# Performance work log

Hardware: AMD Instinct MI355X
Metric: run time of the kernel (lower is better)

## Reference

```python
import jax, jax.numpy as jnp
import numpy as np

N = 100000
IN_DIM = 512
OUT_DIM = 512


def setup_inputs() -> dict:
    key = jax.random.key(0)
    k1, k2, k3, k4 = jax.random.split(key, 4)
    x = jax.random.normal(k1, (N, IN_DIM), dtype=jnp.float32)
    edge_index = jax.random.randint(k2, (2, N), 0, N, dtype=jnp.int64)
    # Linear params (torch nn.Linear: out = x @ W.T + b)
    bound = 1.0 / np.sqrt(IN_DIM)
    W = jax.random.uniform(k3, (OUT_DIM, IN_DIM), minval=-bound, maxval=bound, dtype=jnp.float32)
    b = jax.random.uniform(k4, (OUT_DIM,), minval=-bound, maxval=bound, dtype=jnp.float32)
    return {"x": x, "edge_index": edge_index, "W": W, "b": b}


def reference(x, edge_index, W, b):
    # out = relu(linear(x))
    out = jax.nn.relu(jnp.einsum('ni,oi->no', x, W) + b)  # [N, OUT_DIM]
    # torch.scatter_add(out, 0, col[:, None], x):
    # index has shape [E, 1] so only column 0 of src (= x) is scattered:
    # out[col[e], 0] += x[e, 0]
    col = edge_index[1].astype(jnp.int32)  # [E], E == N here
    E = col.shape[0]
    out = out.at[col, 0].add(x[:E, 0])
    return out
```

## Files before the change

### kernel.cpp

```cpp
#include <hip/hip_runtime.h>
#include <stdint.h>

#define K_DIM 512
#define N_OUT 512
#define BM 128
#define BN 128
#define BK 64

typedef __bf16 bf16x8 __attribute__((ext_vector_type(8)));
typedef float f32x4 __attribute__((ext_vector_type(4)));
typedef unsigned short ushort8 __attribute__((ext_vector_type(8)));

__device__ inline unsigned short f2bf(float f) {
  unsigned u = __float_as_uint(f);
  u += 0x7fffu + ((u >> 16) & 1u);
  return (unsigned short)(u >> 16);
}

__global__ __launch_bounds__(256) void prep_kernel(const float* __restrict__ W,
                                                   unsigned short* __restrict__ wb,
                                                   float* __restrict__ s,
                                                   int n8w, int M) {
  int i = blockIdx.x * 256 + threadIdx.x;
  if (i < n8w) {
    const float4* sp = (const float4*)W + (size_t)i * 2;
    float4 a = sp[0], c = sp[1];
    ushort8 o;
    o[0] = f2bf(a.x); o[1] = f2bf(a.y); o[2] = f2bf(a.z); o[3] = f2bf(a.w);
    o[4] = f2bf(c.x); o[5] = f2bf(c.y); o[6] = f2bf(c.z); o[7] = f2bf(c.w);
    *(ushort8*)(wb + (size_t)i * 8) = o;
  } else {
    int j = i - n8w;
    if (j < M) s[j] = 0.f;
  }
}

__global__ __launch_bounds__(256) void scatter_s_kernel(const float* __restrict__ x,
                                                        const int* __restrict__ ei,
                                                        float* __restrict__ s, int E) {
  int e = blockIdx.x * 256 + threadIdx.x;
  if (e < E) {
    int c = ei[E + e];
    atomicAdd(s + c, x[(size_t)e * K_DIM]);
  }
}

__global__ __launch_bounds__(256) void gemm_fused2_kernel(
    const float* __restrict__ x, const unsigned short* __restrict__ wb,
    const float* __restrict__ b, const float* __restrict__ s,
    float* __restrict__ out, int M) {
  __shared__ __align__(16) unsigned short Als[2][BM * BK];
  __shared__ __align__(16) unsigned short Bls[2][BN * BK];

  const int tid = threadIdx.x;
  const int lane = tid & 63;
  const int quad = lane >> 4;
  const int l16 = lane & 15;
  const int waveId = tid >> 6;
  const int wm = (waveId >> 1) * 64;
  const int wn = (waveId & 1) * 64;

  const int nwg = gridDim.x * gridDim.y;
  int raw = blockIdx.y * gridDim.x + blockIdx.x;
  int q = nwg >> 3, r = nwg & 7;
  int xcd = raw & 7;
  int wg = (xcd < r ? xcd * (q + 1) : r * (q + 1) + (xcd - r) * q) + (raw >> 3);
  const int blockM = (wg >> 2) * BM;
  const int blockN = (wg & 3) * BN;

  size_t goffA[4], goffB[4];
  int ldsoff[4];
#pragma unroll
  for (int i = 0; i < 4; ++i) {
    int ch = i * 256 + tid;
    int row = ch >> 3;
    int c8 = ch & 7;
    int sc = c8 ^ (row & 7);
    int ga_row = blockM + row;
    if (ga_row > M - 1) ga_row = M - 1;
    goffA[i] = (size_t)ga_row * K_DIM + sc * 8;
    goffB[i] = (size_t)(blockN + row) * K_DIM + sc * 8;
    ldsoff[i] = ch * 8;
  }

  f32x4 acc[4][4] = {};
  float4 a0[4], a1[4];

#pragma unroll
  for (int i = 0; i < 4; ++i) {
    __builtin_amdgcn_global_load_lds(
        (const __attribute__((address_space(1))) void*)(wb + goffB[i]),
        (__attribute__((address_space(3))) void*)(&Bls[0][ldsoff[i]]), 16, 0, 0);
    a0[i] = *(const float4*)(x + goffA[i]);
    a1[i] = *(const float4*)(x + goffA[i] + 4);
  }
#pragma unroll
  for (int i = 0; i < 4; ++i) {
    ushort8 o;
    o[0] = f2bf(a0[i].x); o[1] = f2bf(a0[i].y); o[2] = f2bf(a0[i].z); o[3] = f2bf(a0[i].w);
    o[4] = f2bf(a1[i].x); o[5] = f2bf(a1[i].y); o[6] = f2bf(a1[i].z); o[7] = f2bf(a1[i].w);
    *(ushort8*)(&Als[0][ldsoff[i]]) = o;
  }
  __syncthreads();

  int cur = 0;
  for (int k0 = 0; k0 < K_DIM; k0 += BK) {
    const int nxt = cur ^ 1;
    const bool has_next = (k0 + BK) < K_DIM;

    if (has_next) {
#pragma unroll
      for (int i = 0; i < 4; ++i) {
        __builtin_amdgcn_global_load_lds(
            (const __attribute__((address_space(1))) void*)(wb + goffB[i] + k0 + BK),
            (__attribute__((address_space(3))) void*)(&Bls[nxt][ldsoff[i]]), 16, 0, 0);
      }
#pragma unroll
      for (int i = 0; i < 4; ++i) {
        a0[i] = *(const float4*)(x + goffA[i] + k0 + BK);
        a1[i] = *(const float4*)(x + goffA[i] + k0 + BK + 4);
      }
    }

#pragma unroll
    for (int ss = 0; ss < 2; ++ss) {
      bf16x8 af[4], bfr[4];
#pragma unroll
      for (int mi = 0; mi < 4; ++mi) {
        int rr = wm + mi * 16 + l16;
        int c = (ss * 4 + quad) ^ (rr & 7);
        af[mi] = *(const bf16x8*)(&Als[cur][rr * BK + c * 8]);
      }
#pragma unroll
      for (int ni = 0; ni < 4; ++ni) {
        int rr = wn + ni * 16 + l16;
        int c = (ss * 4 + quad) ^ (rr & 7);
        bfr[ni] = *(const bf16x8*)(&Bls[cur][rr * BK + c * 8]);
      }
#pragma unroll
      for (int mi = 0; mi < 4; ++mi)
#pragma unroll
        for (int ni = 0; ni < 4; ++ni)
          acc[mi][ni] = __builtin_amdgcn_mfma_f32_16x16x32_bf16(af[mi], bfr[ni], acc[mi][ni], 0, 0, 0);
    }

    if (has_next) {
#pragma unroll
      for (int i = 0; i < 4; ++i) {
        ushort8 o;
        o[0] = f2bf(a0[i].x); o[1] = f2bf(a0[i].y); o[2] = f2bf(a0[i].z); o[3] = f2bf(a0[i].w);
        o[4] = f2bf(a1[i].x); o[5] = f2bf(a1[i].y); o[6] = f2bf(a1[i].z); o[7] = f2bf(a1[i].w);
        *(ushort8*)(&Als[nxt][ldsoff[i]]) = o;
      }
    }

    __syncthreads();
    cur = nxt;
  }

#pragma unroll
  for (int ni = 0; ni < 4; ++ni) {
    int gcol = blockN + wn + ni * 16 + l16;
    float bias = b[gcol];
#pragma unroll
    for (int mi = 0; mi < 4; ++mi) {
#pragma unroll
      for (int rr = 0; rr < 4; ++rr) {
        int grow = blockM + wm + mi * 16 + quad * 4 + rr;
        if (grow < M) {
          float v = acc[mi][ni][rr] + bias;
          v = v > 0.f ? v : 0.f;
          if (gcol == 0) v += s[grow];
          __builtin_nontemporal_store(v, out + (size_t)grow * N_OUT + gcol);
        }
      }
    }
  }
}

#define LDS_STRIDE 40
__global__ __launch_bounds__(256) void gemm_fused_kernel(
    const float* __restrict__ x, const float* __restrict__ W,
    const float* __restrict__ b, float* __restrict__ out, int M) {
  __shared__ __align__(16) unsigned short Als[BM * LDS_STRIDE];
  __shared__ __align__(16) unsigned short Bls[BN * LDS_STRIDE];
  const int tid = threadIdx.x;
  const int lane = tid & 63;
  const int quad = lane >> 4;
  const int l16 = lane & 15;
  const int waveId = tid >> 6;
  const int wm = (waveId >> 1) * 64;
  const int wn = (waveId & 1) * 64;
  const int blockM = blockIdx.y * BM;
  const int blockN = blockIdx.x * BN;
  f32x4 acc[4][4] = {};
  for (int k0 = 0; k0 < K_DIM; k0 += 32) {
#pragma unroll
    for (int i = 0; i < 4; ++i) {
      int idx = i * 256 + tid;
      int row = idx >> 3;
      int c4 = idx & 7;
      float4 va = make_float4(0.f, 0.f, 0.f, 0.f);
      int grow = blockM + row;
      if (grow < M) va = *(const float4*)(x + (size_t)grow * K_DIM + k0 + c4 * 4);
      ushort4 ha;
      ha.x = f2bf(va.x); ha.y = f2bf(va.y); ha.z = f2bf(va.z); ha.w = f2bf(va.w);
      *(ushort4*)(&Als[row * LDS_STRIDE + c4 * 4]) = ha;
      float4 vb = *(const float4*)(W + (size_t)(blockN + row) * K_DIM + k0 + c4 * 4);
      ushort4 hb;
      hb.x = f2bf(vb.x); hb.y = f2bf(vb.y); hb.z = f2bf(vb.z); hb.w = f2bf(vb.w);
      *(ushort4*)(&Bls[row * LDS_STRIDE + c4 * 4]) = hb;
    }
    __syncthreads();
    bf16x8 af[4], bfr[4];
#pragma unroll
    for (int mi = 0; mi < 4; ++mi)
      af[mi] = *(const bf16x8*)(&Als[(wm + mi * 16 + l16) * LDS_STRIDE + quad * 8]);
#pragma unroll
    for (int ni = 0; ni < 4; ++ni)
      bfr[ni] = *(const bf16x8*)(&Bls[(wn + ni * 16 + l16) * LDS_STRIDE + quad * 8]);
#pragma unroll
    for (int mi = 0; mi < 4; ++mi)
#pragma unroll
      for (int ni = 0; ni < 4; ++ni)
        acc[mi][ni] = __builtin_amdgcn_mfma_f32_16x16x32_bf16(af[mi], bfr[ni], acc[mi][ni], 0, 0, 0);
    __syncthreads();
  }
#pragma unroll
  for (int ni = 0; ni < 4; ++ni) {
    int gcol = blockN + wn + ni * 16 + l16;
    float bias = b[gcol];
#pragma unroll
    for (int mi = 0; mi < 4; ++mi) {
#pragma unroll
      for (int rr = 0; rr < 4; ++rr) {
        int grow = blockM + wm + mi * 16 + quad * 4 + rr;
        if (grow < M) {
          float v = acc[mi][ni][rr] + bias;
          out[(size_t)grow * N_OUT + gcol] = v > 0.f ? v : 0.f;
        }
      }
    }
  }
}

__global__ void scatter_kernel(const float* __restrict__ x,
                               const int* __restrict__ ei,
                               float* __restrict__ out, int E) {
  int e = blockIdx.x * 256 + threadIdx.x;
  if (e < E) {
    int c = ei[E + e];
    atomicAdd(out + (size_t)c * N_OUT, x[(size_t)e * K_DIM]);
  }
}

extern "C" void kernel_launch(void* const* d_in, const int* in_sizes, int n_in,
                              void* d_out, int out_size, void* d_ws, size_t ws_size,
                              hipStream_t stream) {
  const float* x = (const float*)d_in[0];
  const int* ei = (const int*)d_in[1];
  const float* W = (const float*)d_in[2];
  const float* b = (const float*)d_in[3];
  float* out = (float*)d_out;

  int M = in_sizes[0] / K_DIM;
  int E = in_sizes[1] / 2;

  size_t w_elems = (size_t)N_OUT * K_DIM;
  size_t need = w_elems * 2 + (size_t)M * 4 + 64;

  dim3 grid(N_OUT / BN, (M + BM - 1) / BM);

  if (ws_size >= need) {
    unsigned short* wb = (unsigned short*)d_ws;
    float* s = (float*)((char*)d_ws + w_elems * 2);
    int n8w = (int)(w_elems / 8);
    int prep_total = n8w + M;
    prep_kernel<<<(prep_total + 255) / 256, 256, 0, stream>>>(W, wb, s, n8w, M);
    scatter_s_kernel<<<(E + 255) / 256, 256, 0, stream>>>(x, ei, s, E);
    gemm_fused2_kernel<<<grid, 256, 0, stream>>>(x, wb, b, s, out, M);
  } else {
    gemm_fused_kernel<<<grid, 256, 0, stream>>>(x, W, b, out, M);
    scatter_kernel<<<(E + 255) / 256, 256, 0, stream>>>(x, ei, out, E);
  }
}
```

Baseline: 476.0 us.

## Use full-width 64x512 tiles reading W fragments directly from global memory

```diff
diff --git a/kernel.cpp b/kernel.cpp
--- a/kernel.cpp
+++ b/kernel.cpp
@@ -3,8 +3,7 @@
 
 #define K_DIM 512
 #define N_OUT 512
-#define BM 128
-#define BN 128
+#define BM 64
 #define BK 64
 
 typedef __bf16 bf16x8 __attribute__((ext_vector_type(8)));
@@ -45,13 +44,131 @@
   }
 }
 
-__global__ __launch_bounds__(256) void gemm_fused2_kernel(
+__global__ __launch_bounds__(256) void gemm_fused3_kernel(
     const float* __restrict__ x, const unsigned short* __restrict__ wb,
     const float* __restrict__ b, const float* __restrict__ s,
     float* __restrict__ out, int M) {
   __shared__ __align__(16) unsigned short Als[2][BM * BK];
-  __shared__ __align__(16) unsigned short Bls[2][BN * BK];
-
+
+  const int tid = threadIdx.x;
+  const int lane = tid & 63;
+  const int quad = lane >> 4;
+  const int l16 = lane & 15;
+  const int waveId = tid >> 6;
+  const int wn = waveId * 128;
+  const int blockM = blockIdx.x * BM;
+
+  size_t goffA[2];
+  int ldsoff[2];
+#pragma unroll
+  for (int i = 0; i < 2; ++i) {
+    int ch = i * 256 + tid;
+    int row = ch >> 3;
+    int c8 = ch & 7;
+    int sc = c8 ^ (row & 7);
+    int ga_row = blockM + row;
+    if (ga_row > M - 1) ga_row = M - 1;
+    goffA[i] = (size_t)ga_row * K_DIM + sc * 8;
+    ldsoff[i] = ch * 8;
+  }
+
+  const unsigned short* pB[8];
+#pragma unroll
+  for (int ni = 0; ni < 8; ++ni)
+    pB[ni] = wb + (size_t)(wn + ni * 16 + l16) * K_DIM + quad * 8;
+
+  f32x4 acc[4][8] = {};
+  float4 a0[2], a1[2];
+
+#pragma unroll
+  for (int i = 0; i < 2; ++i) {
+    a0[i] = *(const float4*)(x + goffA[i]);
+    a1[i] = *(const float4*)(x + goffA[i] + 4);
+  }
+#pragma unroll
+  for (int i = 0; i < 2; ++i) {
+    ushort8 o;
+    o[0] = f2bf(a0[i].x); o[1] = f2bf(a0[i].y); o[2] = f2bf(a0[i].z); o[3] = f2bf(a0[i].w);
+    o[4] = f2bf(a1[i].x); o[5] = f2bf(a1[i].y); o[6] = f2bf(a1[i].z); o[7] = f2bf(a1[i].w);
+    *(ushort8*)(&Als[0][ldsoff[i]]) = o;
+  }
+  __syncthreads();
+
+  int cur = 0;
+  for (int k0 = 0; k0 < K_DIM; k0 += BK) {
+    const int nxt = cur ^ 1;
+    const bool has_next = (k0 + BK) < K_DIM;
+
+    if (has_next) {
+#pragma unroll
+      for (int i = 0; i < 2; ++i) {
+        a0[i] = *(const float4*)(x + goffA[i] + k0 + BK);
+        a1[i] = *(const float4*)(x + goffA[i] + k0 + BK + 4);
+      }
+    }
+
+#pragma unroll
+    for (int ss = 0; ss < 2; ++ss) {
+      bf16x8 af[4];
+#pragma unroll
+      for (int mi = 0; mi < 4; ++mi) {
+        int rr = mi * 16 + l16;
+        int c = (ss * 4 + quad) ^ (rr & 7);
+        af[mi] = *(const bf16x8*)(&Als[cur][rr * BK + c * 8]);
+      }
+      bf16x8 bfr[8];
+#pragma unroll
+      for (int ni = 0; ni < 8; ++ni)
+        bfr[ni] = *(const bf16x8*)(pB[ni] + k0 + ss * 32);
+#pragma unroll
+      for (int mi = 0; mi < 4; ++mi)
+#pragma unroll
+        for (int ni = 0; ni < 8; ++ni)
+          acc[mi][ni] = __builtin_amdgcn_mfma_f32_16x16x32_bf16(af[mi], bfr[ni], acc[mi][ni], 0, 0, 0);
+    }
+
+    if (has_next) {
+#pragma unroll
+      for (int i = 0; i < 2; ++i) {
+        ushort8 o;
+        o[0] = f2bf(a0[i].x); o[1] = f2bf(a0[i].y); o[2] = f2bf(a0[i].z); o[3] = f2bf(a0[i].w);
+        o[4] = f2bf(a1[i].x); o[5] = f2bf(a1[i].y); o[6] = f2bf(a1[i].z); o[7] = f2bf(a1[i].w);
+        *(ushort8*)(&Als[nxt][ldsoff[i]]) = o;
+      }
+    }
+
+    __syncthreads();
+    cur = nxt;
+  }
+
+#pragma unroll
+  for (int ni = 0; ni < 8; ++ni) {
+    int gcol = wn + ni * 16 + l16;
+    float bias = b[gcol];
+#pragma unroll
+    for (int mi = 0; mi < 4; ++mi) {
+#pragma unroll
+      for (int rr = 0; rr < 4; ++rr) {
+        int grow = blockM + mi * 16 + quad * 4 + rr;
+        if (grow < M) {
+          float v = acc[mi][ni][rr] + bias;
+          v = v > 0.f ? v : 0.f;
+          if (gcol == 0) v += s[grow];
+          __builtin_nontemporal_store(v, out + (size_t)grow * N_OUT + gcol);
+        }
+      }
+    }
+  }
+}
+
+#define FBM 128
+#define FBN 128
+#define LDS_STRIDE 40
+__global__ __launch_bounds__(256) void gemm_fused_kernel(
+    const float* __restrict__ x, const float* __restrict__ W,
+    const float* __restrict__ b, float* __restrict__ out, int M) {
+  __shared__ __align__(16) unsigned short Als[FBM * LDS_STRIDE];
+  __shared__ __align__(16) unsigned short Bls[FBN * LDS_STRIDE];
   const int tid = threadIdx.x;
   const int lane = tid & 63;
   const int quad = lane >> 4;
@@ -59,140 +176,8 @@
   const int waveId = tid >> 6;
   const int wm = (waveId >> 1) * 64;
   const int wn = (waveId & 1) * 64;
-
-  const int nwg = gridDim.x * gridDim.y;
-  int raw = blockIdx.y * gridDim.x + blockIdx.x;
-  int q = nwg >> 3, r = nwg & 7;
-  int xcd = raw & 7;
-  int wg = (xcd < r ? xcd * (q + 1) : r * (q + 1) + (xcd - r) * q) + (raw >> 3);
-  const int blockM = (wg >> 2) * BM;
-  const int blockN = (wg & 3) * BN;
-
-  size_t goffA[4], goffB[4];
-  int ldsoff[4];
-#pragma unroll
-  for (int i = 0; i < 4; ++i) {
-    int ch = i * 256 + tid;
-    int row = ch >> 3;
-    int c8 = ch & 7;
-    int sc = c8 ^ (row & 7);
-    int ga_row = blockM + row;
-    if (ga_row > M - 1) ga_row = M - 1;
-    goffA[i] = (size_t)ga_row * K_DIM + sc * 8;
-    goffB[i] = (size_t)(blockN + row) * K_DIM + sc * 8;
-    ldsoff[i] = ch * 8;
-  }
-
-  f32x4 acc[4][4] = {};
-  float4 a0[4], a1[4];
-
-#pragma unroll
-  for (int i = 0; i < 4; ++i) {
-    __builtin_amdgcn_global_load_lds(
-        (const __attribute__((address_space(1))) void*)(wb + goffB[i]),
-        (__attribute__((address_space(3))) void*)(&Bls[0][ldsoff[i]]), 16, 0, 0);
-    a0[i] = *(const float4*)(x + goffA[i]);
-    a1[i] = *(const float4*)(x + goffA[i] + 4);
-  }
-#pragma unroll
-  for (int i = 0; i < 4; ++i) {
-    ushort8 o;
-    o[0] = f2bf(a0[i].x); o[1] = f2bf(a0[i].y); o[2] = f2bf(a0[i].z); o[3] = f2bf(a0[i].w);
-    o[4] = f2bf(a1[i].x); o[5] = f2bf(a1[i].y); o[6] = f2bf(a1[i].z); o[7] = f2bf(a1[i].w);
-    *(ushort8*)(&Als[0][ldsoff[i]]) = o;
-  }
-  __syncthreads();
-
-  int cur = 0;
-  for (int k0 = 0; k0 < K_DIM; k0 += BK) {
-    const int nxt = cur ^ 1;
-    const bool has_next = (k0 + BK) < K_DIM;
-
-    if (has_next) {
-#pragma unroll
-      for (int i = 0; i < 4; ++i) {
-        __builtin_amdgcn_global_load_lds(
-            (const __attribute__((address_space(1))) void*)(wb + goffB[i] + k0 + BK),
-            (__attribute__((address_space(3))) void*)(&Bls[nxt][ldsoff[i]]), 16, 0, 0);
-      }
-#pragma unroll
-      for (int i = 0; i < 4; ++i) {
-        a0[i] = *(const float4*)(x + goffA[i] + k0 + BK);
-        a1[i] = *(const float4*)(x + goffA[i] + k0 + BK + 4);
-      }
-    }
-
-#pragma unroll
-    for (int ss = 0; ss < 2; ++ss) {
-      bf16x8 af[4], bfr[4];
-#pragma unroll
-      for (int mi = 0; mi < 4; ++mi) {
-        int rr = wm + mi * 16 + l16;
-        int c = (ss * 4 + quad) ^ (rr & 7);
-        af[mi] = *(const bf16x8*)(&Als[cur][rr * BK + c * 8]);
-      }
-#pragma unroll
-      for (int ni = 0; ni < 4; ++ni) {
-        int rr = wn + ni * 16 + l16;
-        int c = (ss * 4 + quad) ^ (rr & 7);
-        bfr[ni] = *(const bf16x8*)(&Bls[cur][rr * BK + c * 8]);
-      }
-#pragma unroll
-      for (int mi = 0; mi < 4; ++mi)
-#pragma unroll
-        for (int ni = 0; ni < 4; ++ni)
-          acc[mi][ni] = __builtin_amdgcn_mfma_f32_16x16x32_bf16(af[mi], bfr[ni], acc[mi][ni], 0, 0, 0);
-    }
-
-    if (has_next) {
-#pragma unroll
-      for (int i = 0; i < 4; ++i) {
-        ushort8 o;
-        o[0] = f2bf(a0[i].x); o[1] = f2bf(a0[i].y); o[2] = f2bf(a0[i].z); o[3] = f2bf(a0[i].w);
-        o[4] = f2bf(a1[i].x); o[5] = f2bf(a1[i].y); o[6] = f2bf(a1[i].z); o[7] = f2bf(a1[i].w);
-        *(ushort8*)(&Als[nxt][ldsoff[i]]) = o;
-      }
-    }
-
-    __syncthreads();
-    cur = nxt;
-  }
-
-#pragma unroll
-  for (int ni = 0; ni < 4; ++ni) {
-    int gcol = blockN + wn + ni * 16 + l16;
-    float bias = b[gcol];
-#pragma unroll
-    for (int mi = 0; mi < 4; ++mi) {
-#pragma unroll
-      for (int rr = 0; rr < 4; ++rr) {
-        int grow = blockM + wm + mi * 16 + quad * 4 + rr;
-        if (grow < M) {
-          float v = acc[mi][ni][rr] + bias;
-          v = v > 0.f ? v : 0.f;
-          if (gcol == 0) v += s[grow];
-          __builtin_nontemporal_store(v, out + (size_t)grow * N_OUT + gcol);
-        }
-      }
-    }
-  }
-}
-
-#define LDS_STRIDE 40
-__global__ __launch_bounds__(256) void gemm_fused_kernel(
-    const float* __restrict__ x, const float* __restrict__ W,
-    const float* __restrict__ b, float* __restrict__ out, int M) {
-  __shared__ __align__(16) unsigned short Als[BM * LDS_STRIDE];
-  __shared__ __align__(16) unsigned short Bls[BN * LDS_STRIDE];
-  const int tid = threadIdx.x;
-  const int lane = tid & 63;
-  const int quad = lane >> 4;
-  const int l16 = lane & 15;
-  const int waveId = tid >> 6;
-  const int wm = (waveId >> 1) * 64;
-  const int wn = (waveId & 1) * 64;
-  const int blockM = blockIdx.y * BM;
-  const int blockN = blockIdx.x * BN;
+  const int blockM = blockIdx.y * FBM;
+  const int blockN = blockIdx.x * FBN;
   f32x4 acc[4][4] = {};
   for (int k0 = 0; k0 < K_DIM; k0 += 32) {
 #pragma unroll
@@ -269,8 +254,6 @@
   size_t w_elems = (size_t)N_OUT * K_DIM;
   size_t need = w_elems * 2 + (size_t)M * 4 + 64;
 
-  dim3 grid(N_OUT / BN, (M + BM - 1) / BM);
-
   if (ws_size >= need) {
     unsigned short* wb = (unsigned short*)d_ws;
     float* s = (float*)((char*)d_ws + w_elems * 2);
@@ -278,9 +261,11 @@
     int prep_total = n8w + M;
     prep_kernel<<<(prep_total + 255) / 256, 256, 0, stream>>>(W, wb, s, n8w, M);
     scatter_s_kernel<<<(E + 255) / 256, 256, 0, stream>>>(x, ei, s, E);
-    gemm_fused2_kernel<<<grid, 256, 0, stream>>>(x, wb, b, s, out, M);
+    int nblk = (M + BM - 1) / BM;
+    gemm_fused3_kernel<<<nblk, 256, 0, stream>>>(x, wb, b, s, out, M);
   } else {
-    gemm_fused_kernel<<<grid, 256, 0, stream>>>(x, W, b, out, M);
+    dim3 fgrid(N_OUT / FBN, (M + FBM - 1) / FBM);
+    gemm_fused_kernel<<<fgrid, 256, 0, stream>>>(x, W, b, out, M);
     scatter_kernel<<<(E + 255) / 256, 256, 0, stream>>>(x, ei, out, E);
   }
 }
```

New measurement: 542.2 us. +13.9%, slower.

## Deepen GEMM prefetch pipeline with explicit waitcnts and packed bf16 conversion

Applied to the files above, without the earlier changes.

```diff
diff --git a/kernel.cpp b/kernel.cpp
--- a/kernel.cpp
+++ b/kernel.cpp
@@ -6,10 +6,12 @@
 #define BM 128
 #define BN 128
 #define BK 64
+#define NT 8
 
 typedef __bf16 bf16x8 __attribute__((ext_vector_type(8)));
 typedef float f32x4 __attribute__((ext_vector_type(4)));
 typedef unsigned short ushort8 __attribute__((ext_vector_type(8)));
+typedef unsigned int u32x4 __attribute__((ext_vector_type(4)));
 
 __device__ inline unsigned short f2bf(float f) {
   unsigned u = __float_as_uint(f);
@@ -17,21 +19,29 @@
   return (unsigned short)(u >> 16);
 }
 
-__global__ __launch_bounds__(256) void prep_kernel(const float* __restrict__ W,
-                                                   unsigned short* __restrict__ wb,
-                                                   float* __restrict__ s,
-                                                   int n8w, int M) {
+__device__ inline unsigned cvt_pk_bf16(float lo, float hi) {
+  unsigned r;
+  asm("v_cvt_pk_bf16_f32 %0, %1, %2" : "=v"(r) : "v"(lo), "v"(hi));
+  return r;
+}
+
+__global__ __launch_bounds__(256) void prep_w_kernel(const float* __restrict__ W,
+                                                     unsigned short* __restrict__ wb,
+                                                     float* __restrict__ s,
+                                                     int n8w, int n8s) {
   int i = blockIdx.x * 256 + threadIdx.x;
   if (i < n8w) {
-    const float4* sp = (const float4*)W + (size_t)i * 2;
-    float4 a = sp[0], c = sp[1];
+    const f32x4* sp = (const f32x4*)W + (size_t)i * 2;
+    f32x4 a = sp[0], c = sp[1];
     ushort8 o;
-    o[0] = f2bf(a.x); o[1] = f2bf(a.y); o[2] = f2bf(a.z); o[3] = f2bf(a.w);
-    o[4] = f2bf(c.x); o[5] = f2bf(c.y); o[6] = f2bf(c.z); o[7] = f2bf(c.w);
+    o[0] = f2bf(a[0]); o[1] = f2bf(a[1]); o[2] = f2bf(a[2]); o[3] = f2bf(a[3]);
+    o[4] = f2bf(c[0]); o[5] = f2bf(c[1]); o[6] = f2bf(c[2]); o[7] = f2bf(c[3]);
     *(ushort8*)(wb + (size_t)i * 8) = o;
-  } else {
+  } else if (i < n8w + n8s) {
     int j = i - n8w;
-    if (j < M) s[j] = 0.f;
+    f32x4 z = {0.f, 0.f, 0.f, 0.f};
+    *(f32x4*)(s + (size_t)j * 8) = z;
+    *(f32x4*)(s + (size_t)j * 8 + 4) = z;
   }
 }
 
@@ -40,12 +50,11 @@
                                                         float* __restrict__ s, int E) {
   int e = blockIdx.x * 256 + threadIdx.x;
   if (e < E) {
-    int c = ei[E + e];
-    atomicAdd(s + c, x[(size_t)e * K_DIM]);
-  }
-}
-
-__global__ __launch_bounds__(256) void gemm_fused2_kernel(
+    atomicAdd(s + ei[E + e], x[(size_t)e * K_DIM]);
+  }
+}
+
+__global__ __launch_bounds__(256) void gemm_x32_kernel(
     const float* __restrict__ x, const unsigned short* __restrict__ wb,
     const float* __restrict__ b, const float* __restrict__ s,
     float* __restrict__ out, int M) {
@@ -83,44 +92,48 @@
     ldsoff[i] = ch * 8;
   }
 
+#define BSTAGE(buf, k0)                                                              \
+  {                                                                                  \
+    _Pragma("unroll") for (int i = 0; i < 4; ++i) {                                  \
+      __builtin_amdgcn_global_load_lds(                                              \
+          (const __attribute__((address_space(1))) void*)(wb + goffB[i] + (k0)),     \
+          (__attribute__((address_space(3))) void*)(&Bls[buf][ldsoff[i]]), 16, 0, 0);\
+    }                                                                                \
+  }
+#define ALOAD(k0)                                                                    \
+  {                                                                                  \
+    _Pragma("unroll") for (int i = 0; i < 4; ++i) {                                  \
+      a0[i] = *(const f32x4*)(x + goffA[i] + (k0));                                  \
+      a1[i] = *(const f32x4*)(x + goffA[i] + (k0) + 4);                              \
+    }                                                                                \
+  }
+#define ACVT(buf)                                                                    \
+  {                                                                                  \
+    _Pragma("unroll") for (int i = 0; i < 4; ++i) {                                  \
+      u32x4 w;                                                                       \
+      w[0] = cvt_pk_bf16(a0[i][0], a0[i][1]);                                        \
+      w[1] = cvt_pk_bf16(a0[i][2], a0[i][3]);                                        \
+      w[2] = cvt_pk_bf16(a1[i][0], a1[i][1]);                                        \
+      w[3] = cvt_pk_bf16(a1[i][2], a1[i][3]);                                        \
+      *(u32x4*)(&Als[buf][ldsoff[i]]) = w;                                           \
+    }                                                                                \
+  }
+
   f32x4 acc[4][4] = {};
-  float4 a0[4], a1[4];
-
-#pragma unroll
-  for (int i = 0; i < 4; ++i) {
-    __builtin_amdgcn_global_load_lds(
-        (const __attribute__((address_space(1))) void*)(wb + goffB[i]),
-        (__attribute__((address_space(3))) void*)(&Bls[0][ldsoff[i]]), 16, 0, 0);
-    a0[i] = *(const float4*)(x + goffA[i]);
-    a1[i] = *(const float4*)(x + goffA[i] + 4);
-  }
-#pragma unroll
-  for (int i = 0; i < 4; ++i) {
-    ushort8 o;
-    o[0] = f2bf(a0[i].x); o[1] = f2bf(a0[i].y); o[2] = f2bf(a0[i].z); o[3] = f2bf(a0[i].w);
-    o[4] = f2bf(a1[i].x); o[5] = f2bf(a1[i].y); o[6] = f2bf(a1[i].z); o[7] = f2bf(a1[i].w);
-    *(ushort8*)(&Als[0][ldsoff[i]]) = o;
-  }
-  __syncthreads();
-
-  int cur = 0;
-  for (int k0 = 0; k0 < K_DIM; k0 += BK) {
+  f32x4 a0[4], a1[4];
+
+  ALOAD(0);
+  BSTAGE(0, 0);
+  ACVT(0);
+  ALOAD(BK);
+  BSTAGE(1, BK);
+  asm volatile("s_waitcnt vmcnt(12) lgkmcnt(0)" ::: "memory");
+  __builtin_amdgcn_s_barrier();
+
+#pragma unroll
+  for (int t = 0; t < NT; ++t) {
+    const int cur = t & 1;
     const int nxt = cur ^ 1;
-    const bool has_next = (k0 + BK) < K_DIM;
-
-    if (has_next) {
-#pragma unroll
-      for (int i = 0; i < 4; ++i) {
-        __builtin_amdgcn_global_load_lds(
-            (const __attribute__((address_space(1))) void*)(wb + goffB[i] + k0 + BK),
-            (__attribute__((address_space(3))) void*)(&Bls[nxt][ldsoff[i]]), 16, 0, 0);
-      }
-#pragma unroll
-      for (int i = 0; i < 4; ++i) {
-        a0[i] = *(const float4*)(x + goffA[i] + k0 + BK);
-        a1[i] = *(const float4*)(x + goffA[i] + k0 + BK + 4);
-      }
-    }
 
 #pragma unroll
     for (int ss = 0; ss < 2; ++ss) {
@@ -137,26 +150,30 @@
         int c = (ss * 4 + quad) ^ (rr & 7);
         bfr[ni] = *(const bf16x8*)(&Bls[cur][rr * BK + c * 8]);
       }
+      __builtin_amdgcn_s_setprio(1);
 #pragma unroll
       for (int mi = 0; mi < 4; ++mi)
 #pragma unroll
         for (int ni = 0; ni < 4; ++ni)
           acc[mi][ni] = __builtin_amdgcn_mfma_f32_16x16x32_bf16(af[mi], bfr[ni], acc[mi][ni], 0, 0, 0);
-    }
-
-    if (has_next) {
-#pragma unroll
-      for (int i = 0; i < 4; ++i) {
-        ushort8 o;
-        o[0] = f2bf(a0[i].x); o[1] = f2bf(a0[i].y); o[2] = f2bf(a0[i].z); o[3] = f2bf(a0[i].w);
-        o[4] = f2bf(a1[i].x); o[5] = f2bf(a1[i].y); o[6] = f2bf(a1[i].z); o[7] = f2bf(a1[i].w);
-        *(ushort8*)(&Als[nxt][ldsoff[i]]) = o;
-      }
-    }
-
-    __syncthreads();
-    cur = nxt;
-  }
+      __builtin_amdgcn_s_setprio(0);
+    }
+
+    if (t + 1 < NT) ACVT(nxt);
+    if (t + 2 < NT) ALOAD((t + 2) * BK);
+
+    if (t + 2 < NT) {
+      asm volatile("s_waitcnt vmcnt(8) lgkmcnt(0)" ::: "memory");
+    } else if (t + 1 < NT) {
+      asm volatile("s_waitcnt vmcnt(0) lgkmcnt(0)" ::: "memory");
+    }
+    if (t + 1 < NT) __builtin_amdgcn_s_barrier();
+
+    if (t + 2 < NT) BSTAGE(cur, (t + 2) * BK);
+  }
+#undef BSTAGE
+#undef ALOAD
+#undef ACVT
 
 #pragma unroll
   for (int ni = 0; ni < 4; ++ni) {
@@ -267,18 +284,22 @@
   int E = in_sizes[1] / 2;
 
   size_t w_elems = (size_t)N_OUT * K_DIM;
-  size_t need = w_elems * 2 + (size_t)M * 4 + 64;
+  int n8w = (int)(w_elems / 8);
+  int n8s = (M + 7) / 8;
+  size_t s_elems = (size_t)n8s * 8;
+
+  size_t need = w_elems * 2 + s_elems * 4;
 
   dim3 grid(N_OUT / BN, (M + BM - 1) / BM);
 
   if (ws_size >= need) {
     unsigned short* wb = (unsigned short*)d_ws;
     float* s = (float*)((char*)d_ws + w_elems * 2);
-    int n8w = (int)(w_elems / 8);
-    int prep_total = n8w + M;
-    prep_kernel<<<(prep_total + 255) / 256, 256, 0, stream>>>(W, wb, s, n8w, M);
+
+    int ptotal = n8w + n8s;
+    prep_w_kernel<<<(ptotal + 255) / 256, 256, 0, stream>>>(W, wb, s, n8w, n8s);
     scatter_s_kernel<<<(E + 255) / 256, 256, 0, stream>>>(x, ei, s, E);
-    gemm_fused2_kernel<<<grid, 256, 0, stream>>>(x, wb, b, s, out, M);
+    gemm_x32_kernel<<<grid, 256, 0, stream>>>(x, wb, b, s, out, M);
   } else {
     gemm_fused_kernel<<<grid, 256, 0, stream>>>(x, W, b, out, M);
     scatter_kernel<<<(E + 255) / 256, 256, 0, stream>>>(x, ei, out, E);
```

Result: faster. 457.9 us (-3.8%).
